# Optimization experiments

Measured on AMD Instinct MI355X. Metric: run time of the kernel, lower is better.

The kernel has to match this reference:

```python
import jax, jax.numpy as jnp
import numpy as np

MARGIN = 2.0
EPS = 1e-9


def setup_inputs() -> dict:
    key = jax.random.key(0)
    k1, k2 = jax.random.split(key)
    N, D, C = 8192, 128, 50
    outputs = jax.random.normal(k1, (N, D), dtype=jnp.float32)
    labels = jax.random.randint(k2, (N,), 0, C, dtype=jnp.int64)
    return {"outputs": outputs, "labels": labels}


def reference(outputs, labels):
    # Pairwise squared distances via Gram trick: ||xi||^2 + ||xj||^2 - 2 xi.xj
    sq = jnp.sum(outputs * outputs, axis=-1)  # [N]
    gram = outputs @ outputs.T                # [N, N]
    dist_sq = jnp.maximum(sq[:, None] + sq[None, :] - 2.0 * gram, 0.0)

    pos = (labels[:, None] == labels[None, :])  # includes i==j, as in original
    num_pos = jnp.sum(pos)
    num_neg = pos.size - num_pos

    dist_pos = jnp.sum(jnp.where(pos, dist_sq, 0.0))
    hinge = jax.nn.relu(MARGIN - jnp.sqrt(dist_sq + EPS))
    dist_neg = jnp.sum(jnp.where(pos, 0.0, hinge * hinge))

    pos_term = jnp.where(num_pos > 0, 0.5 * dist_pos / num_pos, 0.0)
    neg_term = jnp.where(num_neg > 0, 0.5 * dist_neg / num_neg, 0.0)
    return pos_term + neg_term
```

## Files before the change

kernel.cpp:

```cpp
#include <hip/hip_runtime.h>
#include <math.h>

#define NPTS   8192
#define DDIM   128
#define NBLK   64
#define NTRI   2080

using short8 = __attribute__((ext_vector_type(8))) short;
using f32x4  = __attribute__((ext_vector_type(4))) float;

__device__ __forceinline__ unsigned short f2bf(float f) {
    unsigned int u = __float_as_uint(f);
    u += 0x7fffu + ((u >> 16) & 1u);
    return (unsigned short)(u >> 16);
}
__device__ __forceinline__ float bf2f(unsigned short s) {
    return __uint_as_float(((unsigned int)s) << 16);
}

__device__ __forceinline__ void gld_lds16(const unsigned short* g, unsigned short* l) {
    __builtin_amdgcn_global_load_lds(
        (const __attribute__((address_space(1))) unsigned int*)g,
        (__attribute__((address_space(3))) unsigned int*)l,
        16, 0, 0);
}

__global__ __launch_bounds__(256) void prep_kernel(
    const float* __restrict__ X, unsigned short* __restrict__ Xbf,
    float* __restrict__ sq)
{
    const int wave = threadIdx.x >> 6, lane = threadIdx.x & 63;
    const int row  = blockIdx.x * 4 + wave;
    float2 v = *(const float2*)(X + (size_t)row * DDIM + lane * 2);
    unsigned short a = f2bf(v.x), b = f2bf(v.y);
    float fa = bf2f(a), fb = bf2f(b);
    float s = fa * fa + fb * fb;
    *(ushort2*)(Xbf + (size_t)row * DDIM + lane * 2) = make_ushort2(a, b);
#pragma unroll
    for (int off = 32; off > 0; off >>= 1) s += __shfl_down(s, off);
    if (lane == 0) sq[row] = s;
}

__global__ __launch_bounds__(256) void pair_kernel(
    const unsigned short* __restrict__ Xbf, const int* __restrict__ lab,
    const float* __restrict__ sq, float* __restrict__ slots )
{
    const int k = blockIdx.x;
    int bi = (int)((129.0f - sqrtf((float)(16641 - 8 * k))) * 0.5f);
    if (bi < 0) bi = 0;
    while (64 * (bi + 1) - ((bi + 1) * bi) / 2 <= k) ++bi;
    while (64 * bi - (bi * (bi - 1)) / 2 > k) --bi;
    const int bj = bi + (k - (64 * bi - (bi * (bi - 1)) / 2));

    __shared__ unsigned short tile[4096 * 8];
    __shared__ float sSqA[128], sSqB[128];
    __shared__ int   sLabA[128], sLabB[128];
    __shared__ float rP[4], rN[4];

    const int tid   = threadIdx.x;
    const int rowA0 = bi * 128;
    const int rowB0 = bj * 128;

    {
        const int rloc = tid >> 4;
        const int cswz = ((tid & 15) ^ (rloc & 7)) * 8;
        const unsigned short* gA = Xbf + (size_t)(rowA0 + rloc) * DDIM + cswz;
        const unsigned short* gB = Xbf + (size_t)(rowB0 + rloc) * DDIM + cswz;
        unsigned short* lbase = &tile[(size_t)(tid & ~63) * 8];
#pragma unroll
        for (int i = 0; i < 8; ++i)
            gld_lds16(gA + (size_t)i * 16 * DDIM, lbase + i * 2048);
#pragma unroll
        for (int i = 0; i < 8; ++i)
            gld_lds16(gB + (size_t)i * 16 * DDIM, lbase + 16384 + i * 2048);
    }

    if (tid < 128) {
        sSqA[tid]  = sq[rowA0 + tid];
        sLabA[tid] = lab[rowA0 + tid];
    } else {
        int t = tid - 128;
        sSqB[t]  = sq[rowB0 + t];
        sLabB[t] = lab[rowB0 + t];
    }
    __syncthreads();

    const int wave = tid >> 6, lane = tid & 63;
    const int quad = lane >> 4, rr = lane & 15;
    const int wr = wave >> 1, wc = wave & 1;
    const int r7 = rr & 7;

    const unsigned short* tA = &tile[(size_t)(wr * 64 + rr) * 128];
    const unsigned short* tB = &tile[16384 + (size_t)(wc * 64 + rr) * 128];

    f32x4 acc[4][4];
#pragma unroll
    for (int i = 0; i < 4; ++i)
#pragma unroll
        for (int j = 0; j < 4; ++j)
            acc[i][j] = (f32x4){0.f, 0.f, 0.f, 0.f};

#pragma unroll
    for (int kc = 0; kc < 4; ++kc) {
        const int s = (((kc * 4 + quad) ^ r7)) * 8;
        short8 a[4], b[4];
#pragma unroll
        for (int t = 0; t < 4; ++t)
            a[t] = *(const short8*)(tA + t * 16 * 128 + s);
#pragma unroll
        for (int t = 0; t < 4; ++t)
            b[t] = *(const short8*)(tB + t * 16 * 128 + s);
#pragma unroll
        for (int i = 0; i < 4; ++i)
#pragma unroll
            for (int j = 0; j < 4; ++j)
                acc[i][j] = __builtin_amdgcn_mfma_f32_16x16x32_bf16(a[i], b[j], acc[i][j], 0, 0, 0);
    }

    float sb[4]; int lbv[4];
#pragma unroll
    for (int j = 0; j < 4; ++j) {
        int cl = wc * 64 + j * 16 + rr;
        sb[j] = sSqB[cl];
        lbv[j] = sLabB[cl];
    }

    float posS = 0.f, dmin = 1e30f;
#pragma unroll
    for (int i = 0; i < 4; ++i) {
#pragma unroll
        for (int rg = 0; rg < 4; ++rg) {
            int   rl = wr * 64 + i * 16 + quad * 4 + rg;
            float sa = sSqA[rl];
            int   la = sLabA[rl];
#pragma unroll
            for (int j = 0; j < 4; ++j) {
                float d = fmaxf(sa + sb[j] - 2.0f * acc[i][j][rg], 0.0f);
                bool same = (la == lbv[j]);
                posS += same ? d : 0.f;
                dmin = fminf(dmin, same ? 1e30f : d);
            }
        }
    }

    float negS = 0.f;
    if (__any(dmin + 1e-9f < 4.0f)) {
#pragma unroll
        for (int i = 0; i < 4; ++i) {
#pragma unroll
            for (int rg = 0; rg < 4; ++rg) {
                int   rl = wr * 64 + i * 16 + quad * 4 + rg;
                float sa = sSqA[rl];
                int   la = sLabA[rl];
#pragma unroll
                for (int j = 0; j < 4; ++j) {
                    float d = fmaxf(sa + sb[j] - 2.0f * acc[i][j][rg], 0.0f);
                    float t = fmaxf(2.0f - sqrtf(d + 1e-9f), 0.f);
                    negS += (la == lbv[j]) ? 0.f : t * t;
                }
            }
        }
    }

    const float factor = (bi == bj) ? 1.0f : 2.0f;
    posS *= factor; negS *= factor;

#pragma unroll
    for (int off = 32; off > 0; off >>= 1) {
        posS += __shfl_down(posS, off);
        negS += __shfl_down(negS, off);
    }
    if (lane == 0) { rP[wave] = posS; rN[wave] = negS; }
    __syncthreads();
    if (tid == 0) {
        slots[k]        = rP[0] + rP[1] + rP[2] + rP[3];
        slots[NTRI + k] = rN[0] + rN[1] + rN[2] + rN[3];
    }
}

__global__ __launch_bounds__(1024) void finalize_kernel(
    const float* __restrict__ slots, const int* __restrict__ lab,
    float* __restrict__ out)
{
    __shared__ int   hist[64];
    __shared__ float sP[16], sN[16];
    const int tid = threadIdx.x;
    if (tid < 64) hist[tid] = 0;
    __syncthreads();
    for (int i = tid; i < NPTS; i += 1024) atomicAdd(&hist[lab[i]], 1);

    float p = 0.f, n = 0.f;
    for (int i = tid; i < NTRI; i += 1024) { p += slots[i]; n += slots[NTRI + i]; }
#pragma unroll
    for (int off = 32; off > 0; off >>= 1) {
        p += __shfl_down(p, off);
        n += __shfl_down(n, off);
    }
    const int wave = tid >> 6, lane = tid & 63;
    if (lane == 0) { sP[wave] = p; sN[wave] = n; }
    __syncthreads();
    if (tid == 0) {
        long long np = 0;
        for (int c = 0; c < 64; ++c) np += (long long)hist[c] * hist[c];
        float tp = 0.f, tn = 0.f;
#pragma unroll
        for (int w = 0; w < 16; ++w) { tp += sP[w]; tn += sN[w]; }
        double dnp = (double)np;
        double dnn = (double)NPTS * (double)NPTS - dnp;
        double pt = (dnp > 0.0) ? 0.5 * (double)tp / dnp : 0.0;
        double nt = (dnn > 0.0) ? 0.5 * (double)tn / dnn : 0.0;
        out[0] = (float)(pt + nt);
    }
}

extern "C" void kernel_launch(void* const* d_in, const int* in_sizes, int n_in,
                              void* d_out, int out_size, void* d_ws, size_t ws_size,
                              hipStream_t stream) {
    const float* X   = (const float*)d_in[0];
    const int*   lab = (const int*)d_in[1];
    float*       out = (float*)d_out;

    char* ws = (char*)d_ws;
    unsigned short* Xbf   = (unsigned short*)(ws);
    float*          sq    = (float*)(ws + 2 * 1024 * 1024);
    float*          slots = (float*)(ws + 2 * 1024 * 1024 + 32 * 1024);

    prep_kernel<<<NPTS / 4, 256, 0, stream>>>(X, Xbf, sq);
    pair_kernel<<<NTRI, 256, 0, stream>>>(Xbf, lab, sq, slots);
    finalize_kernel<<<1, 1024, 0, stream>>>(slots, lab, out);
}
```

Baseline: 85.21 us.

## Process four tiles per block with double-buffered LDS prefetch

```diff
diff --git a/kernel.cpp b/kernel.cpp
--- a/kernel.cpp
+++ b/kernel.cpp
@@ -5,6 +5,8 @@
 #define DDIM   128
 #define NBLK   64
 #define NTRI   2080
+#define TPB    4
+#define GRID   (NTRI / TPB)
 
 using short8 = __attribute__((ext_vector_type(8))) short;
 using f32x4  = __attribute__((ext_vector_type(4))) float;
@@ -45,106 +47,113 @@
     const unsigned short* __restrict__ Xbf, const int* __restrict__ lab,
     const float* __restrict__ sq, float* __restrict__ slots )
 {
-    const int k = blockIdx.x;
-    int bi = (int)((129.0f - sqrtf((float)(16641 - 8 * k))) * 0.5f);
+    const int k0 = blockIdx.x * TPB;
+    int bi = (int)((129.0f - sqrtf((float)(16641 - 8 * k0))) * 0.5f);
     if (bi < 0) bi = 0;
-    while (64 * (bi + 1) - ((bi + 1) * bi) / 2 <= k) ++bi;
-    while (64 * bi - (bi * (bi - 1)) / 2 > k) --bi;
-    const int bj = bi + (k - (64 * bi - (bi * (bi - 1)) / 2));
-
-    __shared__ unsigned short tile[4096 * 8];
+    while (64 * (bi + 1) - ((bi + 1) * bi) / 2 <= k0) ++bi;
+    while (64 * bi - (bi * (bi - 1)) / 2 > k0) --bi;
+    int bj = bi + (k0 - (64 * bi - (bi * (bi - 1)) / 2));
+
+    __shared__ unsigned short tile[65536];
     __shared__ float sSqA[128], sSqB[128];
     __shared__ int   sLabA[128], sLabB[128];
     __shared__ float rP[4], rN[4];
 
-    const int tid   = threadIdx.x;
-    const int rowA0 = bi * 128;
-    const int rowB0 = bj * 128;
-
-    {
-        const int rloc = tid >> 4;
-        const int cswz = ((tid & 15) ^ (rloc & 7)) * 8;
-        const unsigned short* gA = Xbf + (size_t)(rowA0 + rloc) * DDIM + cswz;
-        const unsigned short* gB = Xbf + (size_t)(rowB0 + rloc) * DDIM + cswz;
-        unsigned short* lbase = &tile[(size_t)(tid & ~63) * 8];
+    const int tid  = threadIdx.x;
+    const int rloc = tid >> 4;
+    const int cswz = ((tid & 15) ^ (rloc & 7)) * 8;
+    const int lws  = (tid & ~63) * 8;
+
+    auto stage = [&](int row0, int panel) {
+        const unsigned short* g = Xbf + (size_t)(row0 + rloc) * DDIM + cswz;
+        unsigned short* l = &tile[panel * 16384 + lws];
 #pragma unroll
         for (int i = 0; i < 8; ++i)
-            gld_lds16(gA + (size_t)i * 16 * DDIM, lbase + i * 2048);
-#pragma unroll
-        for (int i = 0; i < 8; ++i)
-            gld_lds16(gB + (size_t)i * 16 * DDIM, lbase + 16384 + i * 2048);
-    }
-
-    if (tid < 128) {
-        sSqA[tid]  = sq[rowA0 + tid];
-        sLabA[tid] = lab[rowA0 + tid];
-    } else {
-        int t = tid - 128;
-        sSqB[t]  = sq[rowB0 + t];
-        sLabB[t] = lab[rowB0 + t];
-    }
-    __syncthreads();
+            gld_lds16(g + (size_t)i * 16 * DDIM, l + i * 2048);
+    };
+
+    int aCur = 0;
+    stage(bi * 128, 0);
+    stage(bj * 128, 2);
 
     const int wave = tid >> 6, lane = tid & 63;
     const int quad = lane >> 4, rr = lane & 15;
     const int wr = wave >> 1, wc = wave & 1;
     const int r7 = rr & 7;
 
-    const unsigned short* tA = &tile[(size_t)(wr * 64 + rr) * 128];
-    const unsigned short* tB = &tile[16384 + (size_t)(wc * 64 + rr) * 128];
-
-    f32x4 acc[4][4];
-#pragma unroll
-    for (int i = 0; i < 4; ++i)
-#pragma unroll
-        for (int j = 0; j < 4; ++j)
-            acc[i][j] = (f32x4){0.f, 0.f, 0.f, 0.f};
-
-#pragma unroll
-    for (int kc = 0; kc < 4; ++kc) {
-        const int s = (((kc * 4 + quad) ^ r7)) * 8;
-        short8 a[4], b[4];
-#pragma unroll
-        for (int t = 0; t < 4; ++t)
-            a[t] = *(const short8*)(tA + t * 16 * 128 + s);
-#pragma unroll
-        for (int t = 0; t < 4; ++t)
-            b[t] = *(const short8*)(tB + t * 16 * 128 + s);
+    int bi_c = bi, bj_c = bj;
+
+#pragma unroll
+    for (int t = 0; t < TPB; ++t) {
+        const int rowA0 = bi_c * 128, rowB0 = bj_c * 128;
+
+        float sqv; int labv;
+        {
+            int r = (tid < 128) ? (rowA0 + tid) : (rowB0 + (tid - 128));
+            sqv  = sq[r];
+            labv = lab[r];
+        }
+
+        int bi_n = bi_c, bj_n = bj_c + 1;
+        if (bj_n == NBLK) { bi_n = bi_c + 1; bj_n = bi_n; }
+        int aNext = aCur;
+
+        if (t < TPB - 1) {
+            if (bi_n != bi_c) {
+                aNext = aCur ^ 1;
+                stage(bi_n * 128, aNext);
+                stage(bj_n * 128, 2 + ((t + 1) & 1));
+                asm volatile("s_waitcnt vmcnt(16)" ::: "memory");
+            } else {
+                stage(bj_n * 128, 2 + ((t + 1) & 1));
+                asm volatile("s_waitcnt vmcnt(8)" ::: "memory");
+            }
+        } else {
+            asm volatile("s_waitcnt vmcnt(0)" ::: "memory");
+        }
+
+        if (tid < 128) { sSqA[tid] = sqv;      sLabA[tid] = labv; }
+        else           { sSqB[tid - 128] = sqv; sLabB[tid - 128] = labv; }
+        asm volatile("s_waitcnt lgkmcnt(0)" ::: "memory");
+        __builtin_amdgcn_s_barrier();
+        __builtin_amdgcn_sched_barrier(0);
+
+        const unsigned short* tA = &tile[aCur * 16384 + (size_t)(wr * 64 + rr) * 128];
+        const unsigned short* tB = &tile[(2 + (t & 1)) * 16384 + (size_t)(wc * 64 + rr) * 128];
+
+        f32x4 acc[4][4];
 #pragma unroll
         for (int i = 0; i < 4; ++i)
 #pragma unroll
             for (int j = 0; j < 4; ++j)
-                acc[i][j] = __builtin_amdgcn_mfma_f32_16x16x32_bf16(a[i], b[j], acc[i][j], 0, 0, 0);
-    }
-
-    float sb[4]; int lbv[4];
-#pragma unroll
-    for (int j = 0; j < 4; ++j) {
-        int cl = wc * 64 + j * 16 + rr;
-        sb[j] = sSqB[cl];
-        lbv[j] = sLabB[cl];
-    }
-
-    float posS = 0.f, dmin = 1e30f;
-#pragma unroll
-    for (int i = 0; i < 4; ++i) {
-#pragma unroll
-        for (int rg = 0; rg < 4; ++rg) {
-            int   rl = wr * 64 + i * 16 + quad * 4 + rg;
-            float sa = sSqA[rl];
-            int   la = sLabA[rl];
-#pragma unroll
-            for (int j = 0; j < 4; ++j) {
-                float d = fmaxf(sa + sb[j] - 2.0f * acc[i][j][rg], 0.0f);
-                bool same = (la == lbv[j]);
-                posS += same ? d : 0.f;
-                dmin = fminf(dmin, same ? 1e30f : d);
-            }
-        }
-    }
-
-    float negS = 0.f;
-    if (__any(dmin + 1e-9f < 4.0f)) {
+                acc[i][j] = (f32x4){0.f, 0.f, 0.f, 0.f};
+
+#pragma unroll
+        for (int kc = 0; kc < 4; ++kc) {
+            const int s = (((kc * 4 + quad) ^ r7)) * 8;
+            short8 a[4], b[4];
+#pragma unroll
+            for (int u = 0; u < 4; ++u)
+                a[u] = *(const short8*)(tA + u * 16 * 128 + s);
+#pragma unroll
+            for (int u = 0; u < 4; ++u)
+                b[u] = *(const short8*)(tB + u * 16 * 128 + s);
+#pragma unroll
+            for (int i = 0; i < 4; ++i)
+#pragma unroll
+                for (int j = 0; j < 4; ++j)
+                    acc[i][j] = __builtin_amdgcn_mfma_f32_16x16x32_bf16(a[i], b[j], acc[i][j], 0, 0, 0);
+        }
+
+        float sb[4]; int lbv[4];
+#pragma unroll
+        for (int j = 0; j < 4; ++j) {
+            int cl = wc * 64 + j * 16 + rr;
+            sb[j]  = sSqB[cl];
+            lbv[j] = sLabB[cl];
+        }
+
+        float posS = 0.f, dmin = 1e30f;
 #pragma unroll
         for (int i = 0; i < 4; ++i) {
 #pragma unroll
@@ -155,26 +164,50 @@
 #pragma unroll
                 for (int j = 0; j < 4; ++j) {
                     float d = fmaxf(sa + sb[j] - 2.0f * acc[i][j][rg], 0.0f);
-                    float t = fmaxf(2.0f - sqrtf(d + 1e-9f), 0.f);
-                    negS += (la == lbv[j]) ? 0.f : t * t;
+                    bool same = (la == lbv[j]);
+                    posS += same ? d : 0.f;
+                    dmin = fminf(dmin, same ? 1e30f : d);
                 }
             }
         }
-    }
-
-    const float factor = (bi == bj) ? 1.0f : 2.0f;
-    posS *= factor; negS *= factor;
-
-#pragma unroll
-    for (int off = 32; off > 0; off >>= 1) {
-        posS += __shfl_down(posS, off);
-        negS += __shfl_down(negS, off);
-    }
-    if (lane == 0) { rP[wave] = posS; rN[wave] = negS; }
-    __syncthreads();
-    if (tid == 0) {
-        slots[k]        = rP[0] + rP[1] + rP[2] + rP[3];
-        slots[NTRI + k] = rN[0] + rN[1] + rN[2] + rN[3];
+
+        float negS = 0.f;
+        if (__any(dmin + 1e-9f < 4.0f)) {
+#pragma unroll
+            for (int i = 0; i < 4; ++i) {
+#pragma unroll
+                for (int rg = 0; rg < 4; ++rg) {
+                    int   rl = wr * 64 + i * 16 + quad * 4 + rg;
+                    float sa = sSqA[rl];
+                    int   la = sLabA[rl];
+#pragma unroll
+                    for (int j = 0; j < 4; ++j) {
+                        float d = fmaxf(sa + sb[j] - 2.0f * acc[i][j][rg], 0.0f);
+                        float h = fmaxf(2.0f - sqrtf(d + 1e-9f), 0.f);
+                        negS += (la == lbv[j]) ? 0.f : h * h;
+                    }
+                }
+            }
+        }
+
+        const float factor = (bi_c == bj_c) ? 1.0f : 2.0f;
+        posS *= factor; negS *= factor;
+
+#pragma unroll
+        for (int off = 32; off > 0; off >>= 1) {
+            posS += __shfl_down(posS, off);
+            negS += __shfl_down(negS, off);
+        }
+        if (lane == 0) { rP[wave] = posS; rN[wave] = negS; }
+        asm volatile("s_waitcnt lgkmcnt(0)" ::: "memory");
+        __builtin_amdgcn_s_barrier();
+        __builtin_amdgcn_sched_barrier(0);
+        if (tid == 0) {
+            slots[k0 + t]        = rP[0] + rP[1] + rP[2] + rP[3];
+            slots[NTRI + k0 + t] = rN[0] + rN[1] + rN[2] + rN[3];
+        }
+
+        bi_c = bi_n; bj_c = bj_n; aCur = aNext;
     }
 }
 
@@ -226,6 +259,6 @@
     float*          slots = (float*)(ws + 2 * 1024 * 1024 + 32 * 1024);
 
     prep_kernel<<<NPTS / 4, 256, 0, stream>>>(X, Xbf, sq);
-    pair_kernel<<<NTRI, 256, 0, stream>>>(Xbf, lab, sq, slots);
+    pair_kernel<<<GRID, 256, 0, stream>>>(Xbf, lab, sq, slots);
     finalize_kernel<<<1, 1024, 0, stream>>>(slots, lab, out);
 }
```

Measured after the change: 101.5 us. 19.1% more time.

## Enlarge pair tiles to 256x256 with 512-thread blocks over 528 triangle blocks

Applied to the files above, without the earlier changes.

```diff
diff --git a/kernel.cpp b/kernel.cpp
--- a/kernel.cpp
+++ b/kernel.cpp
@@ -3,8 +3,8 @@
 
 #define NPTS   8192
 #define DDIM   128
-#define NBLK   64
-#define NTRI   2080
+#define NBLK2  32
+#define NTRI2  528
 
 using short8 = __attribute__((ext_vector_type(8))) short;
 using f32x4  = __attribute__((ext_vector_type(4))) float;
@@ -41,61 +41,57 @@
     if (lane == 0) sq[row] = s;
 }
 
-__global__ __launch_bounds__(256) void pair_kernel(
+__global__ __launch_bounds__(512, 2) void pair_kernel(
     const unsigned short* __restrict__ Xbf, const int* __restrict__ lab,
     const float* __restrict__ sq, float* __restrict__ slots )
 {
     const int k = blockIdx.x;
-    int bi = (int)((129.0f - sqrtf((float)(16641 - 8 * k))) * 0.5f);
+    int bi = (int)((65.0f - sqrtf((float)(4225 - 8 * k))) * 0.5f);
     if (bi < 0) bi = 0;
-    while (64 * (bi + 1) - ((bi + 1) * bi) / 2 <= k) ++bi;
-    while (64 * bi - (bi * (bi - 1)) / 2 > k) --bi;
-    const int bj = bi + (k - (64 * bi - (bi * (bi - 1)) / 2));
-
-    __shared__ unsigned short tile[4096 * 8];
-    __shared__ float sSqA[128], sSqB[128];
-    __shared__ int   sLabA[128], sLabB[128];
-    __shared__ float rP[4], rN[4];
+    while (32 * (bi + 1) - ((bi + 1) * bi) / 2 <= k) ++bi;
+    while (32 * bi - (bi * (bi - 1)) / 2 > k) --bi;
+    const int bj = bi + (k - (32 * bi - (bi * (bi - 1)) / 2));
+
+    __shared__ unsigned short tile[65536];
+    __shared__ float sSqA[256], sSqB[256];
+    __shared__ int   sLabA[256], sLabB[256];
+    __shared__ float rP[8], rN[8];
 
     const int tid   = threadIdx.x;
-    const int rowA0 = bi * 128;
-    const int rowB0 = bj * 128;
+    const int rowA0 = bi * 256;
+    const int rowB0 = bj * 256;
 
     {
         const int rloc = tid >> 4;
         const int cswz = ((tid & 15) ^ (rloc & 7)) * 8;
         const unsigned short* gA = Xbf + (size_t)(rowA0 + rloc) * DDIM + cswz;
         const unsigned short* gB = Xbf + (size_t)(rowB0 + rloc) * DDIM + cswz;
-        unsigned short* lbase = &tile[(size_t)(tid & ~63) * 8];
+        unsigned short* lA = &tile[(tid & ~63) * 8];
+        unsigned short* lB = &tile[32768 + (tid & ~63) * 8];
 #pragma unroll
         for (int i = 0; i < 8; ++i)
-            gld_lds16(gA + (size_t)i * 16 * DDIM, lbase + i * 2048);
+            gld_lds16(gA + (size_t)i * 32 * DDIM, lA + i * 4096);
 #pragma unroll
         for (int i = 0; i < 8; ++i)
-            gld_lds16(gB + (size_t)i * 16 * DDIM, lbase + 16384 + i * 2048);
-    }
-
-    if (tid < 128) {
-        sSqA[tid]  = sq[rowA0 + tid];
-        sLabA[tid] = lab[rowA0 + tid];
-    } else {
-        int t = tid - 128;
-        sSqB[t]  = sq[rowB0 + t];
-        sLabB[t] = lab[rowB0 + t];
-    }
+            gld_lds16(gB + (size_t)i * 32 * DDIM, lB + i * 4096);
+    }
+
+    if (tid < 256) { sSqA[tid] = sq[rowA0 + tid];        sLabA[tid] = lab[rowA0 + tid]; }
+    else           { sSqB[tid - 256] = sq[rowB0 + tid - 256];
+                     sLabB[tid - 256] = lab[rowB0 + tid - 256]; }
     __syncthreads();
 
     const int wave = tid >> 6, lane = tid & 63;
     const int quad = lane >> 4, rr = lane & 15;
-    const int wr = wave >> 1, wc = wave & 1;
+    const int wr = wave >> 2, wc = wave & 3;
     const int r7 = rr & 7;
 
-    const unsigned short* tA = &tile[(size_t)(wr * 64 + rr) * 128];
-    const unsigned short* tB = &tile[16384 + (size_t)(wc * 64 + rr) * 128];
-
-    f32x4 acc[4][4];
-#pragma unroll
-    for (int i = 0; i < 4; ++i)
+    const unsigned short* tA = &tile[(size_t)(wr * 128 + rr) * 128];
+    const unsigned short* tB = &tile[32768 + (size_t)(wc * 64 + rr) * 128];
+
+    f32x4 acc[8][4];
+#pragma unroll
+    for (int i = 0; i < 8; ++i)
 #pragma unroll
         for (int j = 0; j < 4; ++j)
             acc[i][j] = (f32x4){0.f, 0.f, 0.f, 0.f};
@@ -103,34 +99,44 @@
 #pragma unroll
     for (int kc = 0; kc < 4; ++kc) {
         const int s = (((kc * 4 + quad) ^ r7)) * 8;
-        short8 a[4], b[4];
-#pragma unroll
-        for (int t = 0; t < 4; ++t)
-            a[t] = *(const short8*)(tA + t * 16 * 128 + s);
-#pragma unroll
-        for (int t = 0; t < 4; ++t)
-            b[t] = *(const short8*)(tB + t * 16 * 128 + s);
+        short8 b4[4];
+#pragma unroll
+        for (int u = 0; u < 4; ++u)
+            b4[u] = *(const short8*)(tB + u * 16 * 128 + s);
+        short8 a0[4];
+#pragma unroll
+        for (int u = 0; u < 4; ++u)
+            a0[u] = *(const short8*)(tA + u * 16 * 128 + s);
 #pragma unroll
         for (int i = 0; i < 4; ++i)
 #pragma unroll
             for (int j = 0; j < 4; ++j)
-                acc[i][j] = __builtin_amdgcn_mfma_f32_16x16x32_bf16(a[i], b[j], acc[i][j], 0, 0, 0);
+                acc[i][j] = __builtin_amdgcn_mfma_f32_16x16x32_bf16(a0[i], b4[j], acc[i][j], 0, 0, 0);
+        short8 a1[4];
+#pragma unroll
+        for (int u = 0; u < 4; ++u)
+            a1[u] = *(const short8*)(tA + (4 + u) * 16 * 128 + s);
+#pragma unroll
+        for (int i = 0; i < 4; ++i)
+#pragma unroll
+            for (int j = 0; j < 4; ++j)
+                acc[4 + i][j] = __builtin_amdgcn_mfma_f32_16x16x32_bf16(a1[i], b4[j], acc[4 + i][j], 0, 0, 0);
     }
 
     float sb[4]; int lbv[4];
 #pragma unroll
     for (int j = 0; j < 4; ++j) {
         int cl = wc * 64 + j * 16 + rr;
-        sb[j] = sSqB[cl];
+        sb[j]  = sSqB[cl];
         lbv[j] = sLabB[cl];
     }
 
     float posS = 0.f, dmin = 1e30f;
 #pragma unroll
-    for (int i = 0; i < 4; ++i) {
+    for (int i = 0; i < 8; ++i) {
 #pragma unroll
         for (int rg = 0; rg < 4; ++rg) {
-            int   rl = wr * 64 + i * 16 + quad * 4 + rg;
+            int   rl = wr * 128 + i * 16 + quad * 4 + rg;
             float sa = sSqA[rl];
             int   la = sLabA[rl];
 #pragma unroll
@@ -146,17 +152,17 @@
     float negS = 0.f;
     if (__any(dmin + 1e-9f < 4.0f)) {
 #pragma unroll
-        for (int i = 0; i < 4; ++i) {
+        for (int i = 0; i < 8; ++i) {
 #pragma unroll
             for (int rg = 0; rg < 4; ++rg) {
-                int   rl = wr * 64 + i * 16 + quad * 4 + rg;
+                int   rl = wr * 128 + i * 16 + quad * 4 + rg;
                 float sa = sSqA[rl];
                 int   la = sLabA[rl];
 #pragma unroll
                 for (int j = 0; j < 4; ++j) {
                     float d = fmaxf(sa + sb[j] - 2.0f * acc[i][j][rg], 0.0f);
-                    float t = fmaxf(2.0f - sqrtf(d + 1e-9f), 0.f);
-                    negS += (la == lbv[j]) ? 0.f : t * t;
+                    float h = fmaxf(2.0f - sqrtf(d + 1e-9f), 0.f);
+                    negS += (la == lbv[j]) ? 0.f : h * h;
                 }
             }
         }
@@ -173,8 +179,11 @@
     if (lane == 0) { rP[wave] = posS; rN[wave] = negS; }
     __syncthreads();
     if (tid == 0) {
-        slots[k]        = rP[0] + rP[1] + rP[2] + rP[3];
-        slots[NTRI + k] = rN[0] + rN[1] + rN[2] + rN[3];
+        float tp = 0.f, tn = 0.f;
+#pragma unroll
+        for (int w = 0; w < 8; ++w) { tp += rP[w]; tn += rN[w]; }
+        slots[k]         = tp;
+        slots[NTRI2 + k] = tn;
     }
 }
 
@@ -190,7 +199,7 @@
     for (int i = tid; i < NPTS; i += 1024) atomicAdd(&hist[lab[i]], 1);
 
     float p = 0.f, n = 0.f;
-    for (int i = tid; i < NTRI; i += 1024) { p += slots[i]; n += slots[NTRI + i]; }
+    for (int i = tid; i < NTRI2; i += 1024) { p += slots[i]; n += slots[NTRI2 + i]; }
 #pragma unroll
     for (int off = 32; off > 0; off >>= 1) {
         p += __shfl_down(p, off);
@@ -226,6 +235,6 @@
     float*          slots = (float*)(ws + 2 * 1024 * 1024 + 32 * 1024);
 
     prep_kernel<<<NPTS / 4, 256, 0, stream>>>(X, Xbf, sq);
-    pair_kernel<<<NTRI, 256, 0, stream>>>(Xbf, lab, sq, slots);
+    pair_kernel<<<NTRI2, 512, 0, stream>>>(Xbf, lab, sq, slots);
     finalize_kernel<<<1, 1024, 0, stream>>>(slots, lab, out);
 }
```

New measurement: 87.79 us. 3.0% more time.
